# Kernel optimization log

Measured on AMD Instinct MI355X. Metric: run time of the kernel, lower is better.

## Reference

```python
import jax, jax.numpy as jnp
import numpy as np

GROUP = 64  # hardcoded group_size in the module


def setup_inputs() -> dict:
    key = jax.random.key(0)
    ks = jax.random.split(key, 7)
    B, S, K, N, R = 64, 1, 4096, 12288, 32
    G = K // GROUP
    x = jax.random.normal(ks[0], (B, S, K), jnp.float32)
    # int4 weight residual values in [-8, 7]
    q_w = jax.random.randint(ks[1], (N, K), -8, 8, jnp.int32)
    # per-(group, out_channel) positive scales, shape [G, N] as in the module buffer
    wscales = jax.random.uniform(ks[2], (G, N), jnp.float32, 1e-3, 2e-2)
    lora_down = jax.random.normal(ks[3], (K, R), jnp.float32) * 0.02
    lora_up = jax.random.normal(ks[4], (N, R), jnp.float32) * 0.02
    smooth = jax.random.uniform(ks[5], (K,), jnp.float32, 0.5, 2.0)
    bias = jax.random.normal(ks[6], (N,), jnp.float32) * 0.01
    return {"x": x, "q_w": q_w, "wscales": wscales, "lora_down": lora_down,
            "lora_up": lora_up, "smooth": smooth, "bias": bias}


def reference(x, q_w, wscales, lora_down, lora_up, smooth, bias):
    # x: [B, S, K]; q_w: [N, K] int4 values; wscales: [K//64, N]
    B, S, K = x.shape
    G = K // GROUP
    # smoothing divide (per in-channel)
    x_div = x / smooth  # [B, S, K]
    # --- activation W4A4 path: symmetric int4 per-token per-group quantization ---
    xg = x_div.reshape(B, S, G, GROUP)
    ascale = jnp.maximum(jnp.max(jnp.abs(xg), axis=-1) / 7.0, 1e-8)  # [B, S, G]
    xq = jnp.clip(jnp.round(xg / ascale[..., None]), -8.0, 7.0)
    x_deq = (xq * ascale[..., None]).reshape(B, S, K)  # dequantized activation
    # --- dequantize int4 weight residual: w[n,k] = q[n,k] * wscales[k//64, n] ---
    w_deq = q_w.astype(jnp.float32) * jnp.repeat(wscales, GROUP, axis=0).T  # [N, K]
    # main quantized GEMM
    y = jnp.einsum('bsk,nk->bsn', x_deq, w_deq)  # [B, S, N]
    # low-rank SVD branch on the full-precision smoothed activation
    y = y + (x_div @ lora_down) @ lora_up.T
    y = y + bias
    return y
```

## Files before the change

### kernel.cpp

```cpp
#include <hip/hip_runtime.h>
#include <hip/hip_bf16.h>

#define K_DIM 4096
#define N_DIM 12288
#define B_DIM 64
#define G_DIM 64
#define R_DIM 32
#define AS_LD 68

typedef int v4i __attribute__((ext_vector_type(4)));

__global__ __launch_bounds__(256) void quant_kernel(
    const float* __restrict__ x, const float* __restrict__ smooth,
    char* __restrict__ xq, float* __restrict__ ascale) {
    const int b = blockIdx.x >> 4;
    const int gq = blockIdx.x & 15;
    const int w = threadIdx.x >> 6, lane = threadIdx.x & 63;
    const int g = gq * 4 + w;
    const int k = g * 64 + lane;
    const float xd = x[b * K_DIM + k] / smooth[k];
    float a = fabsf(xd);
    #pragma unroll
    for (int off = 32; off; off >>= 1) a = fmaxf(a, __shfl_xor(a, off));
    const float as = fmaxf(a / 7.0f, 1e-8f);
    float q = rintf(xd / as);
    q = fminf(fmaxf(q, -8.0f), 7.0f);
    xq[b * K_DIM + k] = (char)(int)q;
    if (lane == 0) ascale[b * G_DIM + g] = as;
}

__global__ __launch_bounds__(256) void lora_down_kernel(
    const float* __restrict__ x, const float* __restrict__ smooth,
    const float* __restrict__ ld, float* __restrict__ t) {
    const int b = blockIdx.x >> 4;
    const int kc = blockIdx.x & 15;
    const int r = threadIdx.x & 31;
    const int c = threadIdx.x >> 5;
    const int k0 = kc * 256 + c * 32;
    float acc = 0.f;
    #pragma unroll 8
    for (int k = k0; k < k0 + 32; ++k) {
        const float xd = x[b * K_DIM + k] / smooth[k];
        acc += xd * ld[k * R_DIM + r];
    }
    __shared__ float red[256];
    red[threadIdx.x] = acc;
    __syncthreads();
    if (threadIdx.x < 32) {
        float s = 0.f;
        #pragma unroll
        for (int c2 = 0; c2 < 8; ++c2) s += red[c2 * 32 + threadIdx.x];
        atomicAdd(&t[b * R_DIM + threadIdx.x], s);
    }
}

__global__ __launch_bounds__(256) void main_kernel(
    const int* __restrict__ qw, const float* __restrict__ wscales,
    const char* __restrict__ xq, const float* __restrict__ ascale,
    const float* __restrict__ t, const float* __restrict__ lora_up,
    const float* __restrict__ bias, float* __restrict__ out) {
    __shared__ float s_ws[G_DIM * 16];
    __shared__ float s_as[G_DIM * AS_LD];
    __shared__ float s_red[4 * 64 * 16];

    const int n0 = blockIdx.x * 16;
    const int tid = threadIdx.x;

    for (int i = tid; i < G_DIM * 16; i += 256) {
        const int g = i >> 4, j = i & 15;
        s_ws[i] = wscales[g * N_DIM + n0 + j];
    }
    for (int i = tid; i < B_DIM * G_DIM; i += 256) {
        const int b = i >> 6, g = i & 63;
        s_as[g * AS_LD + b] = ascale[i];
    }
    __syncthreads();

    const int w = tid >> 6, lane = tid & 63;
    const int col = lane & 15, quad = lane >> 4;
    const int g0 = w * 16;

    float facc[4][4];
    #pragma unroll
    for (int bt = 0; bt < 4; ++bt)
        #pragma unroll
        for (int r = 0; r < 4; ++r) facc[bt][r] = 0.f;

    const v4i zero = {0, 0, 0, 0};
    const int* qbase = qw + (size_t)(n0 + col) * K_DIM + quad * 16;
    const char* xbase = xq + (size_t)col * K_DIM + quad * 16;

    v4i q[4], xa[4];
    {
        const int* p = qbase + g0 * 64;
        q[0] = *(const v4i*)(p);
        q[1] = *(const v4i*)(p + 4);
        q[2] = *(const v4i*)(p + 8);
        q[3] = *(const v4i*)(p + 12);
        #pragma unroll
        for (int bt = 0; bt < 4; ++bt)
            xa[bt] = *(const v4i*)(xbase + (size_t)(bt * 16) * K_DIM + g0 * 64);
    }

    for (int gi = 0; gi < 16; ++gi) {
        const int g = g0 + gi;
        const int gn = g0 + (gi < 15 ? gi + 1 : gi);
        v4i qn[4], xan[4];
        {
            const int* p = qbase + gn * 64;
            qn[0] = *(const v4i*)(p);
            qn[1] = *(const v4i*)(p + 4);
            qn[2] = *(const v4i*)(p + 8);
            qn[3] = *(const v4i*)(p + 12);
            #pragma unroll
            for (int bt = 0; bt < 4; ++bt)
                xan[bt] = *(const v4i*)(xbase + (size_t)(bt * 16) * K_DIM + gn * 64);
        }
        v4i bfrag;
        bfrag.x = (q[0].x & 255) | ((q[0].y & 255) << 8) | ((q[0].z & 255) << 16) | (q[0].w << 24);
        bfrag.y = (q[1].x & 255) | ((q[1].y & 255) << 8) | ((q[1].z & 255) << 16) | (q[1].w << 24);
        bfrag.z = (q[2].x & 255) | ((q[2].y & 255) << 8) | ((q[2].z & 255) << 16) | (q[2].w << 24);
        bfrag.w = (q[3].x & 255) | ((q[3].y & 255) << 8) | ((q[3].z & 255) << 16) | (q[3].w << 24);
        const float wsc = s_ws[g * 16 + col];
        #pragma unroll
        for (int bt = 0; bt < 4; ++bt) {
            const v4i d = __builtin_amdgcn_mfma_i32_16x16x64_i8(xa[bt], bfrag, zero, 0, 0, 0);
            const float4 as4 = *(const float4*)&s_as[g * AS_LD + bt * 16 + quad * 4];
            facc[bt][0] = fmaf(as4.x * wsc, (float)d[0], facc[bt][0]);
            facc[bt][1] = fmaf(as4.y * wsc, (float)d[1], facc[bt][1]);
            facc[bt][2] = fmaf(as4.z * wsc, (float)d[2], facc[bt][2]);
            facc[bt][3] = fmaf(as4.w * wsc, (float)d[3], facc[bt][3]);
        }
        #pragma unroll
        for (int j = 0; j < 4; ++j) { q[j] = qn[j]; xa[j] = xan[j]; }
    }

    #pragma unroll
    for (int bt = 0; bt < 4; ++bt)
        #pragma unroll
        for (int r = 0; r < 4; ++r)
            s_red[w * 1024 + lane * 16 + bt * 4 + r] = facc[bt][r];
    __syncthreads();

    #pragma unroll
    for (int i = 0; i < 4; ++i) {
        const int o = tid + i * 256;
        const float v = s_red[o] + s_red[1024 + o] + s_red[2048 + o] + s_red[3072 + o];
        const int lane_o = o >> 4;
        const int bt = (o >> 2) & 3, r = o & 3;
        const int b = bt * 16 + (lane_o >> 4) * 4 + r;
        const int n = n0 + (lane_o & 15);
        float acc = v + bias[n];
        const float4* tp = (const float4*)(t + b * R_DIM);
        const float4* lp = (const float4*)(lora_up + (size_t)n * R_DIM);
        #pragma unroll
        for (int r2 = 0; r2 < R_DIM / 4; ++r2) {
            const float4 tv = tp[r2], lv = lp[r2];
            acc += tv.x * lv.x + tv.y * lv.y + tv.z * lv.z + tv.w * lv.w;
        }
        out[(size_t)b * N_DIM + n] = acc;
    }
}

extern "C" void kernel_launch(void* const* d_in, const int* in_sizes, int n_in,
                              void* d_out, int out_size, void* d_ws, size_t ws_size,
                              hipStream_t stream) {
    const float* x         = (const float*)d_in[0];
    const int*   q_w       = (const int*)d_in[1];
    const float* wscales   = (const float*)d_in[2];
    const float* lora_down = (const float*)d_in[3];
    const float* lora_up   = (const float*)d_in[4];
    const float* smooth    = (const float*)d_in[5];
    const float* bias      = (const float*)d_in[6];
    float* out = (float*)d_out;

    char*  xq     = (char*)d_ws;
    float* ascale = (float*)((char*)d_ws + 262144);
    float* t      = (float*)((char*)d_ws + 262144 + 16384);

    hipMemsetAsync(t, 0, B_DIM * R_DIM * sizeof(float), stream);
    quant_kernel<<<B_DIM * 16, 256, 0, stream>>>(x, smooth, xq, ascale);
    lora_down_kernel<<<B_DIM * 16, 256, 0, stream>>>(x, smooth, lora_down, t);
    main_kernel<<<N_DIM / 16, 256, 0, stream>>>(q_w, wscales, xq, ascale,
                                                t, lora_up, bias, out);
}
```

Baseline: 340.5 us.

## Split main GEMM along K into two blocks per tile with atomic output accumulation

Each 16-column tile of the main kernel is now handled by two blocks that each cover half the K groups. Partial results are combined with atomicAdd into an output zeroed by a new memset, and only the first half adds bias and the LoRA-up term. This doubles the grid (1536 blocks) to fill more CUs for the bandwidth-bound int32 weight stream. It also aliases shared memory to shrink LDS, adds an occupancy hint to launch_bounds, and replaces the manual software prefetch with a fully unrolled loop. The costs are an extra memset over the output, atomic traffic on every output element, and float summation order that is no longer deterministic.

```diff
diff --git a/kernel.cpp b/kernel.cpp
--- a/kernel.cpp
+++ b/kernel.cpp
@@ -54,31 +54,34 @@
     }
 }
 
-__global__ __launch_bounds__(256) void main_kernel(
+__global__ __launch_bounds__(256, 4) void main_kernel(
     const int* __restrict__ qw, const float* __restrict__ wscales,
     const char* __restrict__ xq, const float* __restrict__ ascale,
     const float* __restrict__ t, const float* __restrict__ lora_up,
     const float* __restrict__ bias, float* __restrict__ out) {
-    __shared__ float s_ws[G_DIM * 16];
-    __shared__ float s_as[G_DIM * AS_LD];
-    __shared__ float s_red[4 * 64 * 16];
+    __shared__ float smem[4096];
+    float* s_ws = smem;
+    float* s_as = smem + 512;
+    float* s_red = smem;
 
-    const int n0 = blockIdx.x * 16;
+    const int nt = blockIdx.x >> 1;
+    const int ks = blockIdx.x & 1;
+    const int n0 = nt * 16;
     const int tid = threadIdx.x;
 
-    for (int i = tid; i < G_DIM * 16; i += 256) {
+    for (int i = tid; i < 32 * 16; i += 256) {
         const int g = i >> 4, j = i & 15;
-        s_ws[i] = wscales[g * N_DIM + n0 + j];
+        s_ws[i] = wscales[(ks * 32 + g) * N_DIM + n0 + j];
     }
-    for (int i = tid; i < B_DIM * G_DIM; i += 256) {
-        const int b = i >> 6, g = i & 63;
-        s_as[g * AS_LD + b] = ascale[i];
+    for (int i = tid; i < B_DIM * 32; i += 256) {
+        const int b = i >> 5, gg = i & 31;
+        s_as[gg * AS_LD + b] = ascale[b * G_DIM + ks * 32 + gg];
     }
     __syncthreads();
 
     const int w = tid >> 6, lane = tid & 63;
     const int col = lane & 15, quad = lane >> 4;
-    const int g0 = w * 16;
+    const int gl0 = w * 8;
 
     float facc[4][4];
     #pragma unroll
@@ -87,54 +90,37 @@
         for (int r = 0; r < 4; ++r) facc[bt][r] = 0.f;
 
     const v4i zero = {0, 0, 0, 0};
-    const int* qbase = qw + (size_t)(n0 + col) * K_DIM + quad * 16;
-    const char* xbase = xq + (size_t)col * K_DIM + quad * 16;
+    const size_t kstart = (size_t)(ks * 32 + gl0) * 64 + quad * 16;
+    const int* qbase = qw + (size_t)(n0 + col) * K_DIM + kstart;
+    const char* xbase = xq + (size_t)col * K_DIM + kstart;
 
-    v4i q[4], xa[4];
-    {
-        const int* p = qbase + g0 * 64;
-        q[0] = *(const v4i*)(p);
-        q[1] = *(const v4i*)(p + 4);
-        q[2] = *(const v4i*)(p + 8);
-        q[3] = *(const v4i*)(p + 12);
-        #pragma unroll
-        for (int bt = 0; bt < 4; ++bt)
-            xa[bt] = *(const v4i*)(xbase + (size_t)(bt * 16) * K_DIM + g0 * 64);
-    }
-
-    for (int gi = 0; gi < 16; ++gi) {
-        const int g = g0 + gi;
-        const int gn = g0 + (gi < 15 ? gi + 1 : gi);
-        v4i qn[4], xan[4];
-        {
-            const int* p = qbase + gn * 64;
-            qn[0] = *(const v4i*)(p);
-            qn[1] = *(const v4i*)(p + 4);
-            qn[2] = *(const v4i*)(p + 8);
-            qn[3] = *(const v4i*)(p + 12);
-            #pragma unroll
-            for (int bt = 0; bt < 4; ++bt)
-                xan[bt] = *(const v4i*)(xbase + (size_t)(bt * 16) * K_DIM + gn * 64);
-        }
+    #pragma unroll
+    for (int gi = 0; gi < 8; ++gi) {
+        const int* p = qbase + gi * 64;
+        const v4i q0 = *(const v4i*)(p);
+        const v4i q1 = *(const v4i*)(p + 4);
+        const v4i q2 = *(const v4i*)(p + 8);
+        const v4i q3 = *(const v4i*)(p + 12);
         v4i bfrag;
-        bfrag.x = (q[0].x & 255) | ((q[0].y & 255) << 8) | ((q[0].z & 255) << 16) | (q[0].w << 24);
-        bfrag.y = (q[1].x & 255) | ((q[1].y & 255) << 8) | ((q[1].z & 255) << 16) | (q[1].w << 24);
-        bfrag.z = (q[2].x & 255) | ((q[2].y & 255) << 8) | ((q[2].z & 255) << 16) | (q[2].w << 24);
-        bfrag.w = (q[3].x & 255) | ((q[3].y & 255) << 8) | ((q[3].z & 255) << 16) | (q[3].w << 24);
-        const float wsc = s_ws[g * 16 + col];
+        bfrag.x = (q0.x & 255) | ((q0.y & 255) << 8) | ((q0.z & 255) << 16) | (q0.w << 24);
+        bfrag.y = (q1.x & 255) | ((q1.y & 255) << 8) | ((q1.z & 255) << 16) | (q1.w << 24);
+        bfrag.z = (q2.x & 255) | ((q2.y & 255) << 8) | ((q2.z & 255) << 16) | (q2.w << 24);
+        bfrag.w = (q3.x & 255) | ((q3.y & 255) << 8) | ((q3.z & 255) << 16) | (q3.w << 24);
+        const int gl = gl0 + gi;
+        const float wsc = s_ws[gl * 16 + col];
         #pragma unroll
         for (int bt = 0; bt < 4; ++bt) {
-            const v4i d = __builtin_amdgcn_mfma_i32_16x16x64_i8(xa[bt], bfrag, zero, 0, 0, 0);
-            const float4 as4 = *(const float4*)&s_as[g * AS_LD + bt * 16 + quad * 4];
+            const v4i xa = *(const v4i*)(xbase + (size_t)(bt * 16) * K_DIM + gi * 64);
+            const v4i d = __builtin_amdgcn_mfma_i32_16x16x64_i8(xa, bfrag, zero, 0, 0, 0);
+            const float4 as4 = *(const float4*)&s_as[gl * AS_LD + bt * 16 + quad * 4];
             facc[bt][0] = fmaf(as4.x * wsc, (float)d[0], facc[bt][0]);
             facc[bt][1] = fmaf(as4.y * wsc, (float)d[1], facc[bt][1]);
             facc[bt][2] = fmaf(as4.z * wsc, (float)d[2], facc[bt][2]);
             facc[bt][3] = fmaf(as4.w * wsc, (float)d[3], facc[bt][3]);
         }
-        #pragma unroll
-        for (int j = 0; j < 4; ++j) { q[j] = qn[j]; xa[j] = xan[j]; }
     }
 
+    __syncthreads();
     #pragma unroll
     for (int bt = 0; bt < 4; ++bt)
         #pragma unroll
@@ -145,20 +131,23 @@
     #pragma unroll
     for (int i = 0; i < 4; ++i) {
         const int o = tid + i * 256;
-        const float v = s_red[o] + s_red[1024 + o] + s_red[2048 + o] + s_red[3072 + o];
+        float acc = s_red[o] + s_red[1024 + o] + s_red[2048 + o] + s_red[3072 + o];
         const int lane_o = o >> 4;
         const int bt = (o >> 2) & 3, r = o & 3;
         const int b = bt * 16 + (lane_o >> 4) * 4 + r;
         const int n = n0 + (lane_o & 15);
-        float acc = v + bias[n];
-        const float4* tp = (const float4*)(t + b * R_DIM);
-        const float4* lp = (const float4*)(lora_up + (size_t)n * R_DIM);
-        #pragma unroll
-        for (int r2 = 0; r2 < R_DIM / 4; ++r2) {
-            const float4 tv = tp[r2], lv = lp[r2];
-            acc += tv.x * lv.x + tv.y * lv.y + tv.z * lv.z + tv.w * lv.w;
+        if (ks == 0) {
+            float e = bias[n];
+            const float4* tp = (const float4*)(t + b * R_DIM);
+            const float4* lp = (const float4*)(lora_up + (size_t)n * R_DIM);
+            #pragma unroll
+            for (int r2 = 0; r2 < R_DIM / 4; ++r2) {
+                const float4 tv = tp[r2], lv = lp[r2];
+                e += tv.x * lv.x + tv.y * lv.y + tv.z * lv.z + tv.w * lv.w;
+            }
+            acc += e;
         }
-        out[(size_t)b * N_DIM + n] = acc;
+        atomicAdd(&out[(size_t)b * N_DIM + n], acc);
     }
 }
 
@@ -179,8 +168,9 @@
     float* t      = (float*)((char*)d_ws + 262144 + 16384);
 
     hipMemsetAsync(t, 0, B_DIM * R_DIM * sizeof(float), stream);
+    hipMemsetAsync(out, 0, (size_t)B_DIM * N_DIM * sizeof(float), stream);
     quant_kernel<<<B_DIM * 16, 256, 0, stream>>>(x, smooth, xq, ascale);
     lora_down_kernel<<<B_DIM * 16, 256, 0, stream>>>(x, smooth, lora_down, t);
-    main_kernel<<<N_DIM / 16, 256, 0, stream>>>(q_w, wscales, xq, ascale,
-                                                t, lora_up, bias, out);
+    main_kernel<<<N_DIM / 16 * 2, 256, 0, stream>>>(q_w, wscales, xq, ascale,
+                                                    t, lora_up, bias, out);
 }
```

Result: slower. 359.4 us (+5.5%).

## Prepack int4 weights and activations into MFMA fragment layout before GEMM

Applied to the files above, without the earlier changes.

Adds a prepack kernel that converts the int32 weight matrix into packed int8 MFMA B-fragments in the workspace. The quant kernel now writes activations directly in fragment order, so the main kernel issues one coalesced 16-byte load per fragment with no per-iteration packing. The old layout is kept as a fallback when the workspace is too small. The prepack still reads the full int32 weight every call and writes an extra packed copy, which adds memory traffic inside the timed region. Shared memory is also aliased to cut LDS usage, which needs an extra barrier.

```diff
diff --git a/kernel.cpp b/kernel.cpp
--- a/kernel.cpp
+++ b/kernel.cpp
@@ -7,10 +7,36 @@
 #define G_DIM 64
 #define R_DIM 32
 #define AS_LD 68
+#define NT_DIM 768
 
 typedef int v4i __attribute__((ext_vector_type(4)));
 
-__global__ __launch_bounds__(256) void quant_kernel(
+__device__ __forceinline__ int pack4(const v4i a) {
+    return (a.x & 255) | ((a.y & 255) << 8) | ((a.z & 255) << 16) | (a.w << 24);
+}
+
+__global__ __launch_bounds__(256) void quant_packed_kernel(
+    const float* __restrict__ x, const float* __restrict__ smooth,
+    char* __restrict__ xq_p, float* __restrict__ ascale) {
+    const int b = blockIdx.x >> 4;
+    const int gq = blockIdx.x & 15;
+    const int w = threadIdx.x >> 6, lane = threadIdx.x & 63;
+    const int g = gq * 4 + w;
+    const int k = g * 64 + lane;
+    const float xd = x[b * K_DIM + k] / smooth[k];
+    float a = fabsf(xd);
+    #pragma unroll
+    for (int off = 32; off; off >>= 1) a = fmaxf(a, __shfl_xor(a, off));
+    const float as = fmaxf(a / 7.0f, 1e-8f);
+    float q = rintf(xd / as);
+    q = fminf(fmaxf(q, -8.0f), 7.0f);
+    const int bt = b >> 4, b15 = b & 15;
+    const int quad = lane >> 4, kin = lane & 15;
+    xq_p[((((size_t)bt * G_DIM + g) * 64) + quad * 16 + b15) * 16 + kin] = (char)(int)q;
+    if (lane == 0) ascale[b * G_DIM + g] = as;
+}
+
+__global__ __launch_bounds__(256) void quant_flat_kernel(
     const float* __restrict__ x, const float* __restrict__ smooth,
     char* __restrict__ xq, float* __restrict__ ascale) {
     const int b = blockIdx.x >> 4;
@@ -54,16 +80,41 @@
     }
 }
 
-__global__ __launch_bounds__(256) void main_kernel(
-    const int* __restrict__ qw, const float* __restrict__ wscales,
-    const char* __restrict__ xq, const float* __restrict__ ascale,
+__global__ __launch_bounds__(256) void prepack_kernel(
+    const int* __restrict__ qw, v4i* __restrict__ q8) {
+    const int tid = threadIdx.x;
+    const size_t ebase = (size_t)blockIdx.x * 1024;
+    #pragma unroll
+    for (int p = 0; p < 4; ++p) {
+        const size_t e = ebase + p * 256 + tid;
+        const int ntg = (int)(e >> 6);
+        const int l = (int)e & 63;
+        const int nt = ntg >> 6, g = ntg & 63;
+        const int row = nt * 16 + (l & 15);
+        const int k0 = g * 64 + (l >> 4) * 16;
+        const int* s = qw + (size_t)row * K_DIM + k0;
+        const v4i a0 = *(const v4i*)(s);
+        const v4i a1 = *(const v4i*)(s + 4);
+        const v4i a2 = *(const v4i*)(s + 8);
+        const v4i a3 = *(const v4i*)(s + 12);
+        v4i o;
+        o.x = pack4(a0); o.y = pack4(a1); o.z = pack4(a2); o.w = pack4(a3);
+        q8[e] = o;
+    }
+}
+
+__global__ __launch_bounds__(256) void main_packed_kernel(
+    const v4i* __restrict__ q8, const float* __restrict__ wscales,
+    const v4i* __restrict__ xq_p, const float* __restrict__ ascale,
     const float* __restrict__ t, const float* __restrict__ lora_up,
     const float* __restrict__ bias, float* __restrict__ out) {
-    __shared__ float s_ws[G_DIM * 16];
-    __shared__ float s_as[G_DIM * AS_LD];
-    __shared__ float s_red[4 * 64 * 16];
-
-    const int n0 = blockIdx.x * 16;
+    __shared__ float smem[5440];
+    float* s_ws = smem;
+    float* s_as = smem + 1024;
+    float* s_red = smem;
+
+    const int nt = blockIdx.x;
+    const int n0 = nt * 16;
     const int tid = threadIdx.x;
 
     for (int i = tid; i < G_DIM * 16; i += 256) {
@@ -87,54 +138,27 @@
         for (int r = 0; r < 4; ++r) facc[bt][r] = 0.f;
 
     const v4i zero = {0, 0, 0, 0};
-    const int* qbase = qw + (size_t)(n0 + col) * K_DIM + quad * 16;
-    const char* xbase = xq + (size_t)col * K_DIM + quad * 16;
-
-    v4i q[4], xa[4];
-    {
-        const int* p = qbase + g0 * 64;
-        q[0] = *(const v4i*)(p);
-        q[1] = *(const v4i*)(p + 4);
-        q[2] = *(const v4i*)(p + 8);
-        q[3] = *(const v4i*)(p + 12);
-        #pragma unroll
-        for (int bt = 0; bt < 4; ++bt)
-            xa[bt] = *(const v4i*)(xbase + (size_t)(bt * 16) * K_DIM + g0 * 64);
-    }
-
+    const v4i* qptr = q8 + ((size_t)nt * G_DIM + g0) * 64 + lane;
+    const v4i* xptr = xq_p + (size_t)g0 * 64 + lane;
+
+    #pragma unroll
     for (int gi = 0; gi < 16; ++gi) {
         const int g = g0 + gi;
-        const int gn = g0 + (gi < 15 ? gi + 1 : gi);
-        v4i qn[4], xan[4];
-        {
-            const int* p = qbase + gn * 64;
-            qn[0] = *(const v4i*)(p);
-            qn[1] = *(const v4i*)(p + 4);
-            qn[2] = *(const v4i*)(p + 8);
-            qn[3] = *(const v4i*)(p + 12);
-            #pragma unroll
-            for (int bt = 0; bt < 4; ++bt)
-                xan[bt] = *(const v4i*)(xbase + (size_t)(bt * 16) * K_DIM + gn * 64);
-        }
-        v4i bfrag;
-        bfrag.x = (q[0].x & 255) | ((q[0].y & 255) << 8) | ((q[0].z & 255) << 16) | (q[0].w << 24);
-        bfrag.y = (q[1].x & 255) | ((q[1].y & 255) << 8) | ((q[1].z & 255) << 16) | (q[1].w << 24);
-        bfrag.z = (q[2].x & 255) | ((q[2].y & 255) << 8) | ((q[2].z & 255) << 16) | (q[2].w << 24);
-        bfrag.w = (q[3].x & 255) | ((q[3].y & 255) << 8) | ((q[3].z & 255) << 16) | (q[3].w << 24);
+        const v4i bq = qptr[gi * 64];
         const float wsc = s_ws[g * 16 + col];
         #pragma unroll
         for (int bt = 0; bt < 4; ++bt) {
-            const v4i d = __builtin_amdgcn_mfma_i32_16x16x64_i8(xa[bt], bfrag, zero, 0, 0, 0);
+            const v4i xa = xptr[((size_t)bt * G_DIM + gi) * 64];
+            const v4i d = __builtin_amdgcn_mfma_i32_16x16x64_i8(xa, bq, zero, 0, 0, 0);
             const float4 as4 = *(const float4*)&s_as[g * AS_LD + bt * 16 + quad * 4];
             facc[bt][0] = fmaf(as4.x * wsc, (float)d[0], facc[bt][0]);
             facc[bt][1] = fmaf(as4.y * wsc, (float)d[1], facc[bt][1]);
             facc[bt][2] = fmaf(as4.z * wsc, (float)d[2], facc[bt][2]);
             facc[bt][3] = fmaf(as4.w * wsc, (float)d[3], facc[bt][3]);
         }
-        #pragma unroll
-        for (int j = 0; j < 4; ++j) { q[j] = qn[j]; xa[j] = xan[j]; }
-    }
-
+    }
+
+    __syncthreads();
     #pragma unroll
     for (int bt = 0; bt < 4; ++bt)
         #pragma unroll
@@ -145,12 +169,102 @@
     #pragma unroll
     for (int i = 0; i < 4; ++i) {
         const int o = tid + i * 256;
-        const float v = s_red[o] + s_red[1024 + o] + s_red[2048 + o] + s_red[3072 + o];
+        float acc = s_red[o] + s_red[1024 + o] + s_red[2048 + o] + s_red[3072 + o];
         const int lane_o = o >> 4;
         const int bt = (o >> 2) & 3, r = o & 3;
         const int b = bt * 16 + (lane_o >> 4) * 4 + r;
         const int n = n0 + (lane_o & 15);
-        float acc = v + bias[n];
+        acc += bias[n];
+        const float4* tp = (const float4*)(t + b * R_DIM);
+        const float4* lp = (const float4*)(lora_up + (size_t)n * R_DIM);
+        #pragma unroll
+        for (int r2 = 0; r2 < R_DIM / 4; ++r2) {
+            const float4 tv = tp[r2], lv = lp[r2];
+            acc += tv.x * lv.x + tv.y * lv.y + tv.z * lv.z + tv.w * lv.w;
+        }
+        out[(size_t)b * N_DIM + n] = acc;
+    }
+}
+
+__global__ __launch_bounds__(256) void main_direct_kernel(
+    const int* __restrict__ qw, const float* __restrict__ wscales,
+    const char* __restrict__ xq, const float* __restrict__ ascale,
+    const float* __restrict__ t, const float* __restrict__ lora_up,
+    const float* __restrict__ bias, float* __restrict__ out) {
+    __shared__ float smem[5440];
+    float* s_ws = smem;
+    float* s_as = smem + 1024;
+    float* s_red = smem;
+
+    const int nt = blockIdx.x;
+    const int n0 = nt * 16;
+    const int tid = threadIdx.x;
+
+    for (int i = tid; i < G_DIM * 16; i += 256) {
+        const int g = i >> 4, j = i & 15;
+        s_ws[i] = wscales[g * N_DIM + n0 + j];
+    }
+    for (int i = tid; i < B_DIM * G_DIM; i += 256) {
+        const int b = i >> 6, g = i & 63;
+        s_as[g * AS_LD + b] = ascale[i];
+    }
+    __syncthreads();
+
+    const int w = tid >> 6, lane = tid & 63;
+    const int col = lane & 15, quad = lane >> 4;
+    const int g0 = w * 16;
+
+    float facc[4][4];
+    #pragma unroll
+    for (int bt = 0; bt < 4; ++bt)
+        #pragma unroll
+        for (int r = 0; r < 4; ++r) facc[bt][r] = 0.f;
+
+    const v4i zero = {0, 0, 0, 0};
+    const int* qbase = qw + (size_t)(n0 + col) * K_DIM + (size_t)g0 * 64 + quad * 16;
+    const char* xbase = xq + (size_t)col * K_DIM + (size_t)g0 * 64 + quad * 16;
+
+    #pragma unroll
+    for (int gi = 0; gi < 16; ++gi) {
+        const int* p = qbase + gi * 64;
+        const v4i q0 = *(const v4i*)(p);
+        const v4i q1 = *(const v4i*)(p + 4);
+        const v4i q2 = *(const v4i*)(p + 8);
+        const v4i q3 = *(const v4i*)(p + 12);
+        v4i bfrag;
+        bfrag.x = pack4(q0); bfrag.y = pack4(q1);
+        bfrag.z = pack4(q2); bfrag.w = pack4(q3);
+        const int g = g0 + gi;
+        const float wsc = s_ws[g * 16 + col];
+        #pragma unroll
+        for (int bt = 0; bt < 4; ++bt) {
+            const v4i xa = *(const v4i*)(xbase + (size_t)(bt * 16) * K_DIM + gi * 64);
+            const v4i d = __builtin_amdgcn_mfma_i32_16x16x64_i8(xa, bfrag, zero, 0, 0, 0);
+            const float4 as4 = *(const float4*)&s_as[g * AS_LD + bt * 16 + quad * 4];
+            facc[bt][0] = fmaf(as4.x * wsc, (float)d[0], facc[bt][0]);
+            facc[bt][1] = fmaf(as4.y * wsc, (float)d[1], facc[bt][1]);
+            facc[bt][2] = fmaf(as4.z * wsc, (float)d[2], facc[bt][2]);
+            facc[bt][3] = fmaf(as4.w * wsc, (float)d[3], facc[bt][3]);
+        }
+    }
+
+    __syncthreads();
+    #pragma unroll
+    for (int bt = 0; bt < 4; ++bt)
+        #pragma unroll
+        for (int r = 0; r < 4; ++r)
+            s_red[w * 1024 + lane * 16 + bt * 4 + r] = facc[bt][r];
+    __syncthreads();
+
+    #pragma unroll
+    for (int i = 0; i < 4; ++i) {
+        const int o = tid + i * 256;
+        float acc = s_red[o] + s_red[1024 + o] + s_red[2048 + o] + s_red[3072 + o];
+        const int lane_o = o >> 4;
+        const int bt = (o >> 2) & 3, r = o & 3;
+        const int b = bt * 16 + (lane_o >> 4) * 4 + r;
+        const int n = n0 + (lane_o & 15);
+        acc += bias[n];
         const float4* tp = (const float4*)(t + b * R_DIM);
         const float4* lp = (const float4*)(lora_up + (size_t)n * R_DIM);
         #pragma unroll
@@ -177,10 +291,21 @@
     char*  xq     = (char*)d_ws;
     float* ascale = (float*)((char*)d_ws + 262144);
     float* t      = (float*)((char*)d_ws + 262144 + 16384);
+    v4i*   q8     = (v4i*)((char*)d_ws + 524288);
+
+    const size_t need = 524288 + (size_t)NT_DIM * G_DIM * 64 * 16;
 
     hipMemsetAsync(t, 0, B_DIM * R_DIM * sizeof(float), stream);
-    quant_kernel<<<B_DIM * 16, 256, 0, stream>>>(x, smooth, xq, ascale);
     lora_down_kernel<<<B_DIM * 16, 256, 0, stream>>>(x, smooth, lora_down, t);
-    main_kernel<<<N_DIM / 16, 256, 0, stream>>>(q_w, wscales, xq, ascale,
-                                                t, lora_up, bias, out);
-}
+
+    if (ws_size >= need) {
+        quant_packed_kernel<<<B_DIM * 16, 256, 0, stream>>>(x, smooth, xq, ascale);
+        prepack_kernel<<<3072, 256, 0, stream>>>(q_w, q8);
+        main_packed_kernel<<<NT_DIM, 256, 0, stream>>>(q8, wscales, (const v4i*)xq,
+                                                       ascale, t, lora_up, bias, out);
+    } else {
+        quant_flat_kernel<<<B_DIM * 16, 256, 0, stream>>>(x, smooth, xq, ascale);
+        main_direct_kernel<<<NT_DIM, 256, 0, stream>>>(q_w, wscales, xq, ascale,
+                                                       t, lora_up, bias, out);
+    }
+}
```

Measured after the change: 346.7 us. No clear change (+1.8%).

## Stage packed weights in LDS, split batch across waves, pre-swizzle quantized activations

Applied to the files above, without the earlier changes.

The main kernel now has all four waves cooperatively load and pack each 256-wide K chunk of int32 weights into double-buffered shared memory with coalesced loads. Each wave then reads the packed fragments from LDS and handles its own 16-row batch tile across all of K, which removes the cross-wave shared-memory reduction. The quant kernel writes activations in an MFMA-fragment-swizzled layout so each lane loads its operand with one contiguous vector read, and the LoRA t vector is cached in LDS. The cost is a __syncthreads per chunk and more LDS use per block.

```diff
diff --git a/kernel.cpp b/kernel.cpp
--- a/kernel.cpp
+++ b/kernel.cpp
@@ -6,13 +6,17 @@
 #define B_DIM 64
 #define G_DIM 64
 #define R_DIM 32
-#define AS_LD 68
+#define NT_DIM 768
 
 typedef int v4i __attribute__((ext_vector_type(4)));
 
-__global__ __launch_bounds__(256) void quant_kernel(
+__device__ __forceinline__ int pack4(const v4i a) {
+    return (a.x & 255) | ((a.y & 255) << 8) | ((a.z & 255) << 16) | (a.w << 24);
+}
+
+__global__ __launch_bounds__(256) void quant_packed_kernel(
     const float* __restrict__ x, const float* __restrict__ smooth,
-    char* __restrict__ xq, float* __restrict__ ascale) {
+    char* __restrict__ xq_p, float* __restrict__ ascale) {
     const int b = blockIdx.x >> 4;
     const int gq = blockIdx.x & 15;
     const int w = threadIdx.x >> 6, lane = threadIdx.x & 63;
@@ -25,7 +29,9 @@
     const float as = fmaxf(a / 7.0f, 1e-8f);
     float q = rintf(xd / as);
     q = fminf(fmaxf(q, -8.0f), 7.0f);
-    xq[b * K_DIM + k] = (char)(int)q;
+    const int bt = b >> 4, b15 = b & 15;
+    const int quad = lane >> 4, kin = lane & 15;
+    xq_p[((((size_t)bt * G_DIM + g) * 64) + quad * 16 + b15) * 16 + kin] = (char)(int)q;
     if (lane == 0) ascale[b * G_DIM + g] = as;
 }
 
@@ -54,109 +60,99 @@
     }
 }
 
-__global__ __launch_bounds__(256) void main_kernel(
+__global__ __launch_bounds__(256) void main_fused_kernel(
     const int* __restrict__ qw, const float* __restrict__ wscales,
-    const char* __restrict__ xq, const float* __restrict__ ascale,
+    const v4i* __restrict__ xq_p, const float* __restrict__ ascale,
     const float* __restrict__ t, const float* __restrict__ lora_up,
     const float* __restrict__ bias, float* __restrict__ out) {
     __shared__ float s_ws[G_DIM * 16];
-    __shared__ float s_as[G_DIM * AS_LD];
-    __shared__ float s_red[4 * 64 * 16];
+    __shared__ float s_as[G_DIM * 68];
+    __shared__ float s_t[B_DIM * R_DIM];
+    __shared__ int   s_qp[2][1088];
 
-    const int n0 = blockIdx.x * 16;
+    const int nt = blockIdx.x;
+    const int n0 = nt * 16;
     const int tid = threadIdx.x;
 
-    for (int i = tid; i < G_DIM * 16; i += 256) {
-        const int g = i >> 4, j = i & 15;
-        s_ws[i] = wscales[g * N_DIM + n0 + j];
-    }
+    const int srow = tid >> 4;
+    const int scol = tid & 15;
+    const int* gptr = qw + (size_t)(n0 + srow) * K_DIM + scol * 4;
+
+    for (int i = tid; i < G_DIM * 16; i += 256)
+        s_ws[i] = wscales[(i >> 4) * N_DIM + n0 + (i & 15)];
     for (int i = tid; i < B_DIM * G_DIM; i += 256) {
         const int b = i >> 6, g = i & 63;
-        s_as[g * AS_LD + b] = ascale[i];
+        s_as[g * 68 + b] = ascale[i];
+    }
+    for (int i = tid; i < B_DIM * R_DIM; i += 256) s_t[i] = t[i];
+
+    {
+        v4i qa[4];
+        #pragma unroll
+        for (int i = 0; i < 4; ++i) qa[i] = *(const v4i*)(gptr + i * 64);
+        #pragma unroll
+        for (int i = 0; i < 4; ++i)
+            s_qp[0][srow * 68 + i * 16 + scol] = pack4(qa[i]);
     }
     __syncthreads();
 
     const int w = tid >> 6, lane = tid & 63;
     const int col = lane & 15, quad = lane >> 4;
-    const int g0 = w * 16;
 
-    float facc[4][4];
-    #pragma unroll
-    for (int bt = 0; bt < 4; ++bt)
+    float facc[4] = {0.f, 0.f, 0.f, 0.f};
+    const v4i zero = {0, 0, 0, 0};
+    const v4i* xbase = xq_p + (size_t)w * G_DIM * 64 + lane;
+    const char* rdbase0 = (const char*)&s_qp[0][0] + col * 272 + quad * 16;
+    const char* rdbase1 = (const char*)&s_qp[1][0] + col * 272 + quad * 16;
+
+    #pragma unroll 2
+    for (int j = 0; j < 16; ++j) {
+        v4i qa[4];
+        if (j < 15) {
+            const int* p = gptr + (j + 1) * 256;
+            #pragma unroll
+            for (int i = 0; i < 4; ++i) qa[i] = *(const v4i*)(p + i * 64);
+        }
+        const char* rd = (j & 1) ? rdbase1 : rdbase0;
         #pragma unroll
-        for (int r = 0; r < 4; ++r) facc[bt][r] = 0.f;
-
-    const v4i zero = {0, 0, 0, 0};
-    const int* qbase = qw + (size_t)(n0 + col) * K_DIM + quad * 16;
-    const char* xbase = xq + (size_t)col * K_DIM + quad * 16;
-
-    v4i q[4], xa[4];
-    {
-        const int* p = qbase + g0 * 64;
-        q[0] = *(const v4i*)(p);
-        q[1] = *(const v4i*)(p + 4);
-        q[2] = *(const v4i*)(p + 8);
-        q[3] = *(const v4i*)(p + 12);
-        #pragma unroll
-        for (int bt = 0; bt < 4; ++bt)
-            xa[bt] = *(const v4i*)(xbase + (size_t)(bt * 16) * K_DIM + g0 * 64);
+        for (int gi = 0; gi < 4; ++gi) {
+            const int g = j * 4 + gi;
+            const v4i bq = *(const v4i*)(rd + gi * 64);
+            const v4i xa = xbase[(size_t)g * 64];
+            const v4i d = __builtin_amdgcn_mfma_i32_16x16x64_i8(xa, bq, zero, 0, 0, 0);
+            const float wsc = s_ws[g * 16 + col];
+            const float4 as4 = *(const float4*)&s_as[g * 68 + w * 16 + quad * 4];
+            facc[0] = fmaf(as4.x * wsc, (float)d[0], facc[0]);
+            facc[1] = fmaf(as4.y * wsc, (float)d[1], facc[1]);
+            facc[2] = fmaf(as4.z * wsc, (float)d[2], facc[2]);
+            facc[3] = fmaf(as4.w * wsc, (float)d[3], facc[3]);
+        }
+        if (j < 15) {
+            int* wb = (j & 1) ? &s_qp[0][0] : &s_qp[1][0];
+            #pragma unroll
+            for (int i = 0; i < 4; ++i)
+                wb[srow * 68 + i * 16 + scol] = pack4(qa[i]);
+        }
+        __syncthreads();
     }
 
-    for (int gi = 0; gi < 16; ++gi) {
-        const int g = g0 + gi;
-        const int gn = g0 + (gi < 15 ? gi + 1 : gi);
-        v4i qn[4], xan[4];
-        {
-            const int* p = qbase + gn * 64;
-            qn[0] = *(const v4i*)(p);
-            qn[1] = *(const v4i*)(p + 4);
-            qn[2] = *(const v4i*)(p + 8);
-            qn[3] = *(const v4i*)(p + 12);
-            #pragma unroll
-            for (int bt = 0; bt < 4; ++bt)
-                xan[bt] = *(const v4i*)(xbase + (size_t)(bt * 16) * K_DIM + gn * 64);
-        }
-        v4i bfrag;
-        bfrag.x = (q[0].x & 255) | ((q[0].y & 255) << 8) | ((q[0].z & 255) << 16) | (q[0].w << 24);
-        bfrag.y = (q[1].x & 255) | ((q[1].y & 255) << 8) | ((q[1].z & 255) << 16) | (q[1].w << 24);
-        bfrag.z = (q[2].x & 255) | ((q[2].y & 255) << 8) | ((q[2].z & 255) << 16) | (q[2].w << 24);
-        bfrag.w = (q[3].x & 255) | ((q[3].y & 255) << 8) | ((q[3].z & 255) << 16) | (q[3].w << 24);
-        const float wsc = s_ws[g * 16 + col];
-        #pragma unroll
-        for (int bt = 0; bt < 4; ++bt) {
-            const v4i d = __builtin_amdgcn_mfma_i32_16x16x64_i8(xa[bt], bfrag, zero, 0, 0, 0);
-            const float4 as4 = *(const float4*)&s_as[g * AS_LD + bt * 16 + quad * 4];
-            facc[bt][0] = fmaf(as4.x * wsc, (float)d[0], facc[bt][0]);
-            facc[bt][1] = fmaf(as4.y * wsc, (float)d[1], facc[bt][1]);
-            facc[bt][2] = fmaf(as4.z * wsc, (float)d[2], facc[bt][2]);
-            facc[bt][3] = fmaf(as4.w * wsc, (float)d[3], facc[bt][3]);
-        }
-        #pragma unroll
-        for (int j = 0; j < 4; ++j) { q[j] = qn[j]; xa[j] = xan[j]; }
-    }
-
-    #pragma unroll
-    for (int bt = 0; bt < 4; ++bt)
-        #pragma unroll
-        for (int r = 0; r < 4; ++r)
-            s_red[w * 1024 + lane * 16 + bt * 4 + r] = facc[bt][r];
-    __syncthreads();
-
-    #pragma unroll
-    for (int i = 0; i < 4; ++i) {
-        const int o = tid + i * 256;
-        const float v = s_red[o] + s_red[1024 + o] + s_red[2048 + o] + s_red[3072 + o];
-        const int lane_o = o >> 4;
-        const int bt = (o >> 2) & 3, r = o & 3;
-        const int b = bt * 16 + (lane_o >> 4) * 4 + r;
-        const int n = n0 + (lane_o & 15);
-        float acc = v + bias[n];
-        const float4* tp = (const float4*)(t + b * R_DIM);
+    const int n = n0 + col;
+    float4 lu[8];
+    {
         const float4* lp = (const float4*)(lora_up + (size_t)n * R_DIM);
         #pragma unroll
-        for (int r2 = 0; r2 < R_DIM / 4; ++r2) {
-            const float4 tv = tp[r2], lv = lp[r2];
-            acc += tv.x * lv.x + tv.y * lv.y + tv.z * lv.z + tv.w * lv.w;
+        for (int i = 0; i < 8; ++i) lu[i] = lp[i];
+    }
+    const float bs = bias[n];
+    #pragma unroll
+    for (int r = 0; r < 4; ++r) {
+        const int b = w * 16 + quad * 4 + r;
+        float acc = facc[r] + bs;
+        #pragma unroll
+        for (int r2 = 0; r2 < 8; ++r2) {
+            const float4 tv = *(const float4*)&s_t[b * R_DIM + r2 * 4];
+            acc += tv.x * lu[r2].x + tv.y * lu[r2].y +
+                   tv.z * lu[r2].z + tv.w * lu[r2].w;
         }
         out[(size_t)b * N_DIM + n] = acc;
     }
@@ -179,8 +175,8 @@
     float* t      = (float*)((char*)d_ws + 262144 + 16384);
 
     hipMemsetAsync(t, 0, B_DIM * R_DIM * sizeof(float), stream);
-    quant_kernel<<<B_DIM * 16, 256, 0, stream>>>(x, smooth, xq, ascale);
+    quant_packed_kernel<<<B_DIM * 16, 256, 0, stream>>>(x, smooth, xq, ascale);
     lora_down_kernel<<<B_DIM * 16, 256, 0, stream>>>(x, smooth, lora_down, t);
-    main_kernel<<<N_DIM / 16, 256, 0, stream>>>(q_w, wscales, xq, ascale,
-                                                t, lora_up, bias, out);
+    main_fused_kernel<<<NT_DIM, 256, 0, stream>>>(q_w, wscales, (const v4i*)xq,
+                                                  ascale, t, lora_up, bias, out);
 }
```

Result: faster. 299.7 us (-12.0%).
